# Performance work log

Measured on AMD Instinct MI355X. Metric: run time of the kernel, lower is better.

The kernel has to match this reference:

```python
import jax, jax.numpy as jnp
import numpy as np

A_CUBIC = -0.5  # Keys cubic-convolution parameter (order-3 spline approximation)


def _cubic(t):
    # Keys cubic interpolation kernel, support (-2, 2)
    at = jnp.abs(t)
    at2 = at * at
    at3 = at2 * at
    a = A_CUBIC
    w_inner = (a + 2.0) * at3 - (a + 3.0) * at2 + 1.0          # |t| <= 1
    w_outer = a * at3 - 5.0 * a * at2 + 8.0 * a * at - 4.0 * a  # 1 < |t| < 2
    return jnp.where(at <= 1.0, w_inner, jnp.where(at < 2.0, w_outer, 0.0))


def _spline_upsample_matrix(n_out, n_ctrl):
    # (n_out, n_ctrl) dense weight matrix interpolating control points to the
    # full-resolution axis with the cubic kernel; edge taps clamped (nearest).
    u = jnp.arange(n_out, dtype=jnp.float32) * (n_ctrl - 1) / (n_out - 1)
    i0 = jnp.floor(u).astype(jnp.int32)
    taps = i0[:, None] + jnp.arange(-1, 3)                      # (n_out, 4)
    w = _cubic(u[:, None] - taps.astype(jnp.float32))           # (n_out, 4)
    taps_c = jnp.clip(taps, 0, n_ctrl - 1)
    B = jnp.zeros((n_out, n_ctrl), jnp.float32)
    B = B.at[jnp.arange(n_out)[:, None], taps_c].add(w)
    return B


def _elastic_warp(img, displacement):
    # img: (H, W, C); displacement: (2, 3, 3) control-point displacements (dy, dx)
    H, W, C = img.shape
    By = _spline_upsample_matrix(H, displacement.shape[1])      # (H, 3)
    Bx = _spline_upsample_matrix(W, displacement.shape[2])      # (W, 3)
    disp = jnp.einsum('hy,dyx,wx->dhw', By, displacement, Bx)   # (2, H, W)

    yy = jnp.arange(H, dtype=jnp.float32)[:, None] + disp[0]    # sample coords
    xx = jnp.arange(W, dtype=jnp.float32)[None, :] + disp[1]
    iy0 = jnp.floor(yy).astype(jnp.int32)
    ix0 = jnp.floor(xx).astype(jnp.int32)

    out = jnp.zeros_like(img)
    # 4x4 cubic tap stencil (fixed small loop; each iteration is one full gather)
    for a in range(-1, 3):
        ty = iy0 + a
        wy = _cubic(yy - ty.astype(jnp.float32))                # (H, W)
        tyc = jnp.clip(ty, 0, H - 1)
        for b in range(-1, 3):
            tx = ix0 + b
            wx = _cubic(xx - tx.astype(jnp.float32))            # (H, W)
            txc = jnp.clip(tx, 0, W - 1)
            out = out + (wy * wx)[..., None] * img[tyc, txc]    # gather (H,W,C)
    return out


def setup_inputs() -> dict:
    key = jax.random.key(0)
    k1, k2 = jax.random.split(key)
    H, W, C = 2048, 4096, 3
    inputs = jax.random.normal(k1, (H, W, C), dtype=jnp.float32)
    displacement = jax.random.normal(k2, (2, 3, 3), dtype=jnp.float32)
    return {"inputs": inputs, "displacement": displacement}


def reference(inputs, displacement):
    # module draws displacement ~ N(0,1)*5 internally; externalized here
    return _elastic_warp(inputs, displacement * 5.0)
```

## Files before the change

kernel.cpp:

```cpp
#include <hip/hip_runtime.h>
#include <math.h>

constexpr int H = 2048;
constexpr int W = 4096;
constexpr int RS = W * 3;

__device__ __forceinline__ float k_inner(float t) {
    return fmaf(fmaf(1.5f, t, -2.5f), t * t, 1.0f);
}
__device__ __forceinline__ float k_outer(float t) {
    return fmaf(fmaf(fmaf(-0.5f, t, 2.5f), t, -4.0f), t, 2.0f);
}
__device__ __forceinline__ float cubic_w(float t) {
    float at = fabsf(t);
    if (at <= 1.0f) return k_inner(at);
    if (at < 2.0f)  return k_outer(at);
    return 0.0f;
}

__global__ __launch_bounds__(256, 4)
void elastic_warp_kernel(const float* __restrict__ img,
                         const float* __restrict__ dctrl,
                         float* __restrict__ out) {
    int h = blockIdx.x >> 4;
    int w = ((blockIdx.x & 15) << 8) | threadIdx.x;

    __shared__ float s_cy[6];
    if (threadIdx.x == 0) {
        float u = (float)(2 * h) / (float)(H - 1);
        float i0 = floorf(u);
        float by0 = 0.0f, by1 = 0.0f, by2 = 0.0f;
#pragma unroll
        for (int k = -1; k < 3; ++k) {
            float tap = i0 + (float)k;
            float wt = cubic_w(u - tap);
            int tc = (int)tap;
            tc = tc < 0 ? 0 : (tc > 2 ? 2 : tc);
            if (tc == 0) by0 += wt; else if (tc == 1) by1 += wt; else by2 += wt;
        }
#pragma unroll
        for (int x = 0; x < 3; ++x) {
            s_cy[x]     = 5.0f * (by0 * dctrl[x]     + by1 * dctrl[3 + x]  + by2 * dctrl[6 + x]);
            s_cy[3 + x] = 5.0f * (by0 * dctrl[9 + x] + by1 * dctrl[12 + x] + by2 * dctrl[15 + x]);
        }
    }
    __syncthreads();

    float u = (float)w * (2.0f / 4095.0f);
    bool hiu = u >= 1.0f;
    float s = u - (hiu ? 1.0f : 0.0f);
    float o1 = k_outer(1.0f + s);
    float is = k_inner(s);
    float i1 = k_inner(1.0f - s);
    float o2 = k_outer(2.0f - s);
    float bx0 = hiu ? o1 : (o1 + is);
    float bx1 = hiu ? is : i1;
    float bx2 = hiu ? (i1 + o2) : o2;

    float d0 = s_cy[0] * bx0 + s_cy[1] * bx1 + s_cy[2] * bx2;
    float d1 = s_cy[3] * bx0 + s_cy[4] * bx1 + s_cy[5] * bx2;

    float yy = (float)h + d0;
    float xx = (float)w + d1;
    float iy0f = floorf(yy);
    float ix0f = floorf(xx);
    float fy = yy - iy0f;
    float fx = xx - ix0f;
    int iy0 = (int)iy0f;
    int ix0 = (int)ix0f;

    float wy0 = k_outer(1.0f + fy), wy1 = k_inner(fy), wy2 = k_inner(1.0f - fy), wy3 = k_outer(2.0f - fy);
    float wx0 = k_outer(1.0f + fx), wx1 = k_inner(fx), wx2 = k_inner(1.0f - fx), wx3 = k_outer(2.0f - fx);
    float wy[4] = {wy0, wy1, wy2, wy3};

    float acc0 = 0.0f, acc1 = 0.0f, acc2 = 0.0f;

    bool interior = (iy0 >= 1) & (iy0 <= H - 3) & (ix0 >= 1) & (ix0 <= W - 3);
    if (interior) {
        int off = ((iy0 - 1) * W + (ix0 - 1)) * 3;

        float4 v[4][3];
#pragma unroll
        for (int a = 0; a < 4; ++a) {
            const float4* p = (const float4*)(img + off + a * RS);
            v[a][0] = p[0];
            v[a][1] = p[1];
            v[a][2] = p[2];
        }

#pragma unroll
        for (int a = 0; a < 4; ++a) {
            float q0 = wy[a] * wx0, q1 = wy[a] * wx1, q2 = wy[a] * wx2, q3 = wy[a] * wx3;
            float4 va = v[a][0], vb = v[a][1], vc = v[a][2];
            acc0 = fmaf(q0, va.x, fmaf(q1, va.w, fmaf(q2, vb.z, fmaf(q3, vc.y, acc0))));
            acc1 = fmaf(q0, va.y, fmaf(q1, vb.x, fmaf(q2, vb.w, fmaf(q3, vc.z, acc1))));
            acc2 = fmaf(q0, va.z, fmaf(q1, vb.y, fmaf(q2, vc.x, fmaf(q3, vc.w, acc2))));
        }
    } else {
        float wx[4] = {wx0, wx1, wx2, wx3};
#pragma unroll
        for (int a = 0; a < 4; ++a) {
            int ty = iy0 + a - 1;
            ty = ty < 0 ? 0 : (ty > H - 1 ? H - 1 : ty);
            int rowoff = ty * RS;
            float ay = wy[a];
#pragma unroll
            for (int b = 0; b < 4; ++b) {
                int tx = ix0 + b - 1;
                tx = tx < 0 ? 0 : (tx > W - 1 ? W - 1 : tx);
                float wgt = ay * wx[b];
                const float* p = img + rowoff + tx * 3;
                acc0 += wgt * p[0];
                acc1 += wgt * p[1];
                acc2 += wgt * p[2];
            }
        }
    }

    int oo = (blockIdx.x * 256 + threadIdx.x) * 3;
    out[oo + 0] = acc0;
    out[oo + 1] = acc1;
    out[oo + 2] = acc2;
}

extern "C" void kernel_launch(void* const* d_in, const int* in_sizes, int n_in,
                              void* d_out, int out_size, void* d_ws, size_t ws_size,
                              hipStream_t stream) {
    const float* img   = (const float*)d_in[0];
    const float* dctrl = (const float*)d_in[1];
    float* out = (float*)d_out;

    int blocks = (H * W) / 256;
    elastic_warp_kernel<<<blocks, 256, 0, stream>>>(img, dctrl, out);
}
```

Measured before the change: 66.85 us.

## Process two adjacent pixels per thread sharing a 6x6 stencil load

Each thread now computes two horizontally adjacent output pixels and loads one shared 6-row by 6-pixel window, with per-pixel weights shifted into that window according to the relative offsets. This is meant to cut redundant global loads between overlapping stencils and halve the thread count. The fast path runs only when every lane in the wavefront meets the offset and bounds conditions; otherwise all lanes fall back to two scalar clamped gathers. Output stores become float2 writes. The risks are higher register pressure, since the occupancy hint was dropped from launch bounds, and extra FMAs against zero weights.

```diff
diff --git a/kernel.cpp b/kernel.cpp
--- a/kernel.cpp
+++ b/kernel.cpp
@@ -18,18 +18,42 @@
     return 0.0f;
 }
 
-__global__ __launch_bounds__(256, 4)
+__device__ __forceinline__ void gather_px(const float* __restrict__ img,
+                                          int iy, int ix,
+                                          const float wy[4], const float wx[4],
+                                          float& o0, float& o1, float& o2) {
+    o0 = 0.f; o1 = 0.f; o2 = 0.f;
+#pragma unroll
+    for (int a = 0; a < 4; ++a) {
+        int ty = iy + a - 1;
+        ty = ty < 0 ? 0 : (ty > H - 1 ? H - 1 : ty);
+        int rowoff = ty * RS;
+        float ay = wy[a];
+#pragma unroll
+        for (int b = 0; b < 4; ++b) {
+            int tx = ix + b - 1;
+            tx = tx < 0 ? 0 : (tx > W - 1 ? W - 1 : tx);
+            float wgt = ay * wx[b];
+            const float* p = img + rowoff + tx * 3;
+            o0 += wgt * p[0];
+            o1 += wgt * p[1];
+            o2 += wgt * p[2];
+        }
+    }
+}
+
+__global__ __launch_bounds__(256)
 void elastic_warp_kernel(const float* __restrict__ img,
                          const float* __restrict__ dctrl,
                          float* __restrict__ out) {
-    int h = blockIdx.x >> 4;
-    int w = ((blockIdx.x & 15) << 8) | threadIdx.x;
+    int h  = blockIdx.x >> 3;
+    int x0 = ((blockIdx.x & 7) << 9) | ((int)threadIdx.x << 1);
 
     __shared__ float s_cy[6];
     if (threadIdx.x == 0) {
         float u = (float)(2 * h) / (float)(H - 1);
         float i0 = floorf(u);
-        float by0 = 0.0f, by1 = 0.0f, by2 = 0.0f;
+        float by0 = 0.f, by1 = 0.f, by2 = 0.f;
 #pragma unroll
         for (int k = -1; k < 3; ++k) {
             float tap = i0 + (float)k;
@@ -45,82 +69,118 @@
         }
     }
     __syncthreads();
+    float cy0 = s_cy[0], cy1 = s_cy[1], cy2 = s_cy[2];
+    float cy3 = s_cy[3], cy4 = s_cy[4], cy5 = s_cy[5];
 
-    float u = (float)w * (2.0f / 4095.0f);
-    bool hiu = u >= 1.0f;
-    float s = u - (hiu ? 1.0f : 0.0f);
-    float o1 = k_outer(1.0f + s);
-    float is = k_inner(s);
-    float i1 = k_inner(1.0f - s);
-    float o2 = k_outer(2.0f - s);
-    float bx0 = hiu ? o1 : (o1 + is);
-    float bx1 = hiu ? is : i1;
-    float bx2 = hiu ? (i1 + o2) : o2;
+    float d0[2], d1[2];
+#pragma unroll
+    for (int p = 0; p < 2; ++p) {
+        float u = (float)(x0 + p) * (2.0f / 4095.0f);
+        bool hiu = u >= 1.0f;
+        float s = u - (hiu ? 1.0f : 0.0f);
+        float o1v = k_outer(1.0f + s);
+        float isv = k_inner(s);
+        float i1v = k_inner(1.0f - s);
+        float o2v = k_outer(2.0f - s);
+        float bx0 = hiu ? o1v : (o1v + isv);
+        float bx1 = hiu ? isv : i1v;
+        float bx2 = hiu ? (i1v + o2v) : o2v;
+        d0[p] = cy0 * bx0 + cy1 * bx1 + cy2 * bx2;
+        d1[p] = cy3 * bx0 + cy4 * bx1 + cy5 * bx2;
+    }
 
-    float d0 = s_cy[0] * bx0 + s_cy[1] * bx1 + s_cy[2] * bx2;
-    float d1 = s_cy[3] * bx0 + s_cy[4] * bx1 + s_cy[5] * bx2;
+    float yy0 = (float)h + d0[0],  xx0 = (float)x0 + d1[0];
+    float yy1 = (float)h + d0[1],  xx1 = (float)(x0 + 1) + d1[1];
+    float fly0 = floorf(yy0), flx0 = floorf(xx0);
+    float fly1 = floorf(yy1), flx1 = floorf(xx1);
+    float fy0 = yy0 - fly0, fx0 = xx0 - flx0;
+    float fy1 = yy1 - fly1, fx1 = xx1 - flx1;
+    int iy0 = (int)fly0, ix0 = (int)flx0;
+    int iy1 = (int)fly1, ix1 = (int)flx1;
 
-    float yy = (float)h + d0;
-    float xx = (float)w + d1;
-    float iy0f = floorf(yy);
-    float ix0f = floorf(xx);
-    float fy = yy - iy0f;
-    float fx = xx - ix0f;
-    int iy0 = (int)iy0f;
-    int ix0 = (int)ix0f;
+    float wy0[4] = {k_outer(1.f + fy0), k_inner(fy0), k_inner(1.f - fy0), k_outer(2.f - fy0)};
+    float wx0[4] = {k_outer(1.f + fx0), k_inner(fx0), k_inner(1.f - fx0), k_outer(2.f - fx0)};
+    float wy1[4] = {k_outer(1.f + fy1), k_inner(fy1), k_inner(1.f - fy1), k_outer(2.f - fy1)};
+    float wx1[4] = {k_outer(1.f + fx1), k_inner(fx1), k_inner(1.f - fx1), k_outer(2.f - fx1)};
 
-    float wy0 = k_outer(1.0f + fy), wy1 = k_inner(fy), wy2 = k_inner(1.0f - fy), wy3 = k_outer(2.0f - fy);
-    float wx0 = k_outer(1.0f + fx), wx1 = k_inner(fx), wx2 = k_inner(1.0f - fx), wx3 = k_outer(2.0f - fx);
-    float wy[4] = {wy0, wy1, wy2, wy3};
+    float a0, a1, a2, b0, b1, b2;
 
-    float acc0 = 0.0f, acc1 = 0.0f, acc2 = 0.0f;
+    int e  = ix1 - ix0;
+    int f1 = iy1 - iy0 + 1;
+    bool fast = (iy0 >= 2) & (iy0 <= H - 4) & (ix0 >= 1) & (ix0 <= W - 5) &
+                (e >= 0) & (e <= 2) & (f1 >= 0) & (f1 <= 2);
 
-    bool interior = (iy0 >= 1) & (iy0 <= H - 3) & (ix0 >= 1) & (ix0 <= W - 3);
-    if (interior) {
-        int off = ((iy0 - 1) * W + (ix0 - 1)) * 3;
+    if (__all(fast)) {
+        int br = iy0 - 2;
+        int bc3 = (ix0 - 1) * 3;
 
-        float4 v[4][3];
-#pragma unroll
-        for (int a = 0; a < 4; ++a) {
-            const float4* p = (const float4*)(img + off + a * RS);
-            v[a][0] = p[0];
-            v[a][1] = p[1];
-            v[a][2] = p[2];
-        }
+        bool e0 = (e == 0), e1 = (e == 1);
+        float wx1d[6];
+        wx1d[0] = e0 ? wx1[0] : 0.f;
+        wx1d[1] = e0 ? wx1[1] : (e1 ? wx1[0] : 0.f);
+        wx1d[2] = e0 ? wx1[2] : (e1 ? wx1[1] : wx1[0]);
+        wx1d[3] = e0 ? wx1[3] : (e1 ? wx1[2] : wx1[1]);
+        wx1d[4] = e0 ? 0.f    : (e1 ? wx1[3] : wx1[2]);
+        wx1d[5] = (!e0 && !e1) ? wx1[3] : 0.f;
+
+        bool f0 = (f1 == 0), fo = (f1 == 1);
+        float wr1[6];
+        wr1[0] = f0 ? wy1[0] : 0.f;
+        wr1[1] = f0 ? wy1[1] : (fo ? wy1[0] : 0.f);
+        wr1[2] = f0 ? wy1[2] : (fo ? wy1[1] : wy1[0]);
+        wr1[3] = f0 ? wy1[3] : (fo ? wy1[2] : wy1[1]);
+        wr1[4] = f0 ? 0.f    : (fo ? wy1[3] : wy1[2]);
+        wr1[5] = (!f0 && !fo) ? wy1[3] : 0.f;
+
+        a0 = a1 = a2 = 0.f;
+        b0 = b1 = b2 = 0.f;
 
 #pragma unroll
-        for (int a = 0; a < 4; ++a) {
-            float q0 = wy[a] * wx0, q1 = wy[a] * wx1, q2 = wy[a] * wx2, q3 = wy[a] * wx3;
-            float4 va = v[a][0], vb = v[a][1], vc = v[a][2];
-            acc0 = fmaf(q0, va.x, fmaf(q1, va.w, fmaf(q2, vb.z, fmaf(q3, vc.y, acc0))));
-            acc1 = fmaf(q0, va.y, fmaf(q1, vb.x, fmaf(q2, vb.w, fmaf(q3, vc.z, acc1))));
-            acc2 = fmaf(q0, va.z, fmaf(q1, vb.y, fmaf(q2, vc.x, fmaf(q3, vc.w, acc2))));
+        for (int r = 0; r < 6; ++r) {
+            const float* rp = img + (br + r) * RS + bc3;
+            float4 A = *(const float4*)(rp);
+            float4 B = *(const float4*)(rp + 4);
+            float4 Cc = *(const float4*)(rp + 8);
+            float4 E = *(const float4*)(rp + 12);
+            float2 Dd = *(const float2*)(rp + 16);
+            float v0 = A.x,  v1 = A.y,  v2 = A.z,  v3 = A.w;
+            float v4 = B.x,  v5 = B.y,  v6 = B.z,  v7 = B.w;
+            float v8 = Cc.x, v9 = Cc.y, v10 = Cc.z, v11 = Cc.w;
+            float v12 = E.x, v13 = E.y, v14 = E.z, v15 = E.w;
+            float v16 = Dd.x, v17 = Dd.y;
+
+            float s0 = fmaf(wx1d[0], v0,  fmaf(wx1d[1], v3,  fmaf(wx1d[2], v6,
+                       fmaf(wx1d[3], v9,  fmaf(wx1d[4], v12, wx1d[5] * v15)))));
+            float s1 = fmaf(wx1d[0], v1,  fmaf(wx1d[1], v4,  fmaf(wx1d[2], v7,
+                       fmaf(wx1d[3], v10, fmaf(wx1d[4], v13, wx1d[5] * v16)))));
+            float s2 = fmaf(wx1d[0], v2,  fmaf(wx1d[1], v5,  fmaf(wx1d[2], v8,
+                       fmaf(wx1d[3], v11, fmaf(wx1d[4], v14, wx1d[5] * v17)))));
+            b0 = fmaf(wr1[r], s0, b0);
+            b1 = fmaf(wr1[r], s1, b1);
+            b2 = fmaf(wr1[r], s2, b2);
+
+            if (r >= 1 && r <= 4) {
+                float t0 = fmaf(wx0[0], v0, fmaf(wx0[1], v3, fmaf(wx0[2], v6,  wx0[3] * v9)));
+                float t1 = fmaf(wx0[0], v1, fmaf(wx0[1], v4, fmaf(wx0[2], v7,  wx0[3] * v10)));
+                float t2 = fmaf(wx0[0], v2, fmaf(wx0[1], v5, fmaf(wx0[2], v8,  wx0[3] * v11)));
+                float ay = wy0[r - 1];
+                a0 = fmaf(ay, t0, a0);
+                a1 = fmaf(ay, t1, a1);
+                a2 = fmaf(ay, t2, a2);
+            }
         }
     } else {
-        float wx[4] = {wx0, wx1, wx2, wx3};
-#pragma unroll
-        for (int a = 0; a < 4; ++a) {
-            int ty = iy0 + a - 1;
-            ty = ty < 0 ? 0 : (ty > H - 1 ? H - 1 : ty);
-            int rowoff = ty * RS;
-            float ay = wy[a];
-#pragma unroll
-            for (int b = 0; b < 4; ++b) {
-                int tx = ix0 + b - 1;
-                tx = tx < 0 ? 0 : (tx > W - 1 ? W - 1 : tx);
-                float wgt = ay * wx[b];
-                const float* p = img + rowoff + tx * 3;
-                acc0 += wgt * p[0];
-                acc1 += wgt * p[1];
-                acc2 += wgt * p[2];
-            }
-        }
+        gather_px(img, iy0, ix0, wy0, wx0, a0, a1, a2);
+        gather_px(img, iy1, ix1, wy1, wx1, b0, b1, b2);
     }
 
-    int oo = (blockIdx.x * 256 + threadIdx.x) * 3;
-    out[oo + 0] = acc0;
-    out[oo + 1] = acc1;
-    out[oo + 2] = acc2;
+    int oo = (h * W + x0) * 3;
+    float2 w01 = {a0, a1};
+    float2 w23 = {a2, b0};
+    float2 w45 = {b1, b2};
+    *(float2*)(out + oo)     = w01;
+    *(float2*)(out + oo + 2) = w23;
+    *(float2*)(out + oo + 4) = w45;
 }
 
 extern "C" void kernel_launch(void* const* d_in, const int* in_sizes, int n_in,
@@ -130,6 +190,6 @@
     const float* dctrl = (const float*)d_in[1];
     float* out = (float*)d_out;
 
-    int blocks = (H * W) / 256;
+    int blocks = H * (W / 512);
     elastic_warp_kernel<<<blocks, 256, 0, stream>>>(img, dctrl, out);
 }
```

Result: slower. 101.4 us (+51.7%).

## Stage 2D image window in LDS and gather cubic taps from shared memory

Applied to the files above, without the earlier changes.

Reshapes blocks from 1x256 rows to 64x4 tiles and cooperatively loads a 12-row by 72-pixel window of the image into shared memory, sized around the block's base displacement. Each thread then reads its 4x4 stencil from LDS instead of issuing unaligned global float4 loads, exploiting the smooth displacement field to reuse neighbouring pixels. A block-wide vote falls back to the clamped global path when any tap lies outside the window. This adds two extra barriers and shared-memory traffic, and lowers occupancy through the launch-bounds change and the LDS footprint.

```diff
diff --git a/kernel.cpp b/kernel.cpp
--- a/kernel.cpp
+++ b/kernel.cpp
@@ -4,6 +4,10 @@
 constexpr int H = 2048;
 constexpr int W = 4096;
 constexpr int RS = W * 3;
+
+constexpr int WIN_ROWS = 12;
+constexpr int WIN_DW   = 216;
+constexpr int WIN_STRIDE = 220;
 
 __device__ __forceinline__ float k_inner(float t) {
     return fmaf(fmaf(1.5f, t, -2.5f), t * t, 1.0f);
@@ -18,34 +22,26 @@
     return 0.0f;
 }
 
-__global__ __launch_bounds__(256, 4)
-void elastic_warp_kernel(const float* __restrict__ img,
-                         const float* __restrict__ dctrl,
-                         float* __restrict__ out) {
-    int h = blockIdx.x >> 4;
-    int w = ((blockIdx.x & 15) << 8) | threadIdx.x;
+__device__ __forceinline__ void row_cy(int h, const float* __restrict__ dctrl, float cy[6]) {
+    float u = (float)(2 * h) / (float)(H - 1);
+    float i0 = floorf(u);
+    float by0 = 0.f, by1 = 0.f, by2 = 0.f;
+#pragma unroll
+    for (int k = -1; k < 3; ++k) {
+        float tap = i0 + (float)k;
+        float wt = cubic_w(u - tap);
+        int tc = (int)tap;
+        tc = tc < 0 ? 0 : (tc > 2 ? 2 : tc);
+        if (tc == 0) by0 += wt; else if (tc == 1) by1 += wt; else by2 += wt;
+    }
+#pragma unroll
+    for (int x = 0; x < 3; ++x) {
+        cy[x]     = 5.0f * (by0 * dctrl[x]     + by1 * dctrl[3 + x]  + by2 * dctrl[6 + x]);
+        cy[3 + x] = 5.0f * (by0 * dctrl[9 + x] + by1 * dctrl[12 + x] + by2 * dctrl[15 + x]);
+    }
+}
 
-    __shared__ float s_cy[6];
-    if (threadIdx.x == 0) {
-        float u = (float)(2 * h) / (float)(H - 1);
-        float i0 = floorf(u);
-        float by0 = 0.0f, by1 = 0.0f, by2 = 0.0f;
-#pragma unroll
-        for (int k = -1; k < 3; ++k) {
-            float tap = i0 + (float)k;
-            float wt = cubic_w(u - tap);
-            int tc = (int)tap;
-            tc = tc < 0 ? 0 : (tc > 2 ? 2 : tc);
-            if (tc == 0) by0 += wt; else if (tc == 1) by1 += wt; else by2 += wt;
-        }
-#pragma unroll
-        for (int x = 0; x < 3; ++x) {
-            s_cy[x]     = 5.0f * (by0 * dctrl[x]     + by1 * dctrl[3 + x]  + by2 * dctrl[6 + x]);
-            s_cy[3 + x] = 5.0f * (by0 * dctrl[9 + x] + by1 * dctrl[12 + x] + by2 * dctrl[15 + x]);
-        }
-    }
-    __syncthreads();
-
+__device__ __forceinline__ void bx3(int w, float& b0, float& b1, float& b2) {
     float u = (float)w * (2.0f / 4095.0f);
     bool hiu = u >= 1.0f;
     float s = u - (hiu ? 1.0f : 0.0f);
@@ -53,50 +49,100 @@
     float is = k_inner(s);
     float i1 = k_inner(1.0f - s);
     float o2 = k_outer(2.0f - s);
-    float bx0 = hiu ? o1 : (o1 + is);
-    float bx1 = hiu ? is : i1;
-    float bx2 = hiu ? (i1 + o2) : o2;
+    b0 = hiu ? o1 : (o1 + is);
+    b1 = hiu ? is : i1;
+    b2 = hiu ? (i1 + o2) : o2;
+}
 
-    float d0 = s_cy[0] * bx0 + s_cy[1] * bx1 + s_cy[2] * bx2;
-    float d1 = s_cy[3] * bx0 + s_cy[4] * bx1 + s_cy[5] * bx2;
+__global__ __launch_bounds__(256)
+void elastic_warp_kernel(const float* __restrict__ img,
+                         const float* __restrict__ dctrl,
+                         float* __restrict__ out) {
+    int x0 = blockIdx.x << 6;
+    int y0 = blockIdx.y << 2;
+    int t = threadIdx.x;
+    int r = t >> 6;
+    int w = x0 + (t & 63);
+    int h = y0 + r;
+
+    __shared__ float s_cy[4][6];
+    __shared__ int   s_base[2];
+    __shared__ int   s_flag[4];
+    __shared__ float s_win[WIN_ROWS][WIN_STRIDE];
+
+    if (t < 4) {
+        float cy[6];
+        row_cy(y0 + t, dctrl, cy);
+#pragma unroll
+        for (int j = 0; j < 6; ++j) s_cy[t][j] = cy[j];
+        if (t == 0) {
+            float b0, b1, b2; bx3(x0, b0, b1, b2);
+            float d0 = cy[0]*b0 + cy[1]*b1 + cy[2]*b2;
+            float d1 = cy[3]*b0 + cy[4]*b1 + cy[5]*b2;
+            s_base[0] = (int)floorf((float)y0 + d0);
+            s_base[1] = (int)floorf((float)x0 + d1);
+        }
+    }
+    __syncthreads();
+
+    float cy0 = s_cy[r][0], cy1 = s_cy[r][1], cy2 = s_cy[r][2];
+    float cy3 = s_cy[r][3], cy4 = s_cy[r][4], cy5 = s_cy[r][5];
+    int base_iy = s_base[0], base_ix = s_base[1];
+
+    float bx0, bx1, bx2; bx3(w, bx0, bx1, bx2);
+    float d0 = cy0*bx0 + cy1*bx1 + cy2*bx2;
+    float d1 = cy3*bx0 + cy4*bx1 + cy5*bx2;
 
     float yy = (float)h + d0;
     float xx = (float)w + d1;
-    float iy0f = floorf(yy);
-    float ix0f = floorf(xx);
-    float fy = yy - iy0f;
-    float fx = xx - ix0f;
-    int iy0 = (int)iy0f;
-    int ix0 = (int)ix0f;
+    float fly = floorf(yy), flx = floorf(xx);
+    float fy = yy - fly, fx = xx - flx;
+    int iy0 = (int)fly, ix0 = (int)flx;
+
+    int yb = base_iy - 2;
+    int xb = (base_ix - 2) & ~3;
+
+    int ry0 = iy0 - 1 - yb;
+    int cxp = ix0 - 1 - xb;
+
+    bool uok = (yb >= 0) & (yb + WIN_ROWS - 1 <= H - 1) & (xb >= 0) & (xb + 71 <= W - 1);
+    bool lok = (ry0 >= 0) & (ry0 <= 8) & (cxp >= 0) & (cxp <= 68);
+    int wflag = __all(uok & lok);
+    if ((t & 63) == 0) s_flag[t >> 6] = wflag;
+    __syncthreads();
+    bool fast = s_flag[0] && s_flag[1] && s_flag[2] && s_flag[3];
 
     float wy0 = k_outer(1.0f + fy), wy1 = k_inner(fy), wy2 = k_inner(1.0f - fy), wy3 = k_outer(2.0f - fy);
     float wx0 = k_outer(1.0f + fx), wx1 = k_inner(fx), wx2 = k_inner(1.0f - fx), wx3 = k_outer(2.0f - fx);
-    float wy[4] = {wy0, wy1, wy2, wy3};
 
-    float acc0 = 0.0f, acc1 = 0.0f, acc2 = 0.0f;
+    float acc0 = 0.f, acc1 = 0.f, acc2 = 0.f;
 
-    bool interior = (iy0 >= 1) & (iy0 <= H - 3) & (ix0 >= 1) & (ix0 <= W - 3);
-    if (interior) {
-        int off = ((iy0 - 1) * W + (ix0 - 1)) * 3;
+    if (fast) {
+        const float* gbase = img + yb * RS + xb * 3;
+#pragma unroll
+        for (int it = 0; it < 3; ++it) {
+            int idx = t + (it << 8);
+            if (idx < 648) {
+                int row = idx / 54;
+                int c4  = idx - row * 54;
+                float4 v = *(const float4*)(gbase + row * RS + (c4 << 2));
+                *(float4*)&s_win[row][c4 << 2] = v;
+            }
+        }
+        __syncthreads();
 
-        float4 v[4][3];
+        int cxd = cxp * 3;
+        float wyA[4] = {wy0, wy1, wy2, wy3};
 #pragma unroll
         for (int a = 0; a < 4; ++a) {
-            const float4* p = (const float4*)(img + off + a * RS);
-            v[a][0] = p[0];
-            v[a][1] = p[1];
-            v[a][2] = p[2];
-        }
-
-#pragma unroll
-        for (int a = 0; a < 4; ++a) {
-            float q0 = wy[a] * wx0, q1 = wy[a] * wx1, q2 = wy[a] * wx2, q3 = wy[a] * wx3;
-            float4 va = v[a][0], vb = v[a][1], vc = v[a][2];
-            acc0 = fmaf(q0, va.x, fmaf(q1, va.w, fmaf(q2, vb.z, fmaf(q3, vc.y, acc0))));
-            acc1 = fmaf(q0, va.y, fmaf(q1, vb.x, fmaf(q2, vb.w, fmaf(q3, vc.z, acc1))));
-            acc2 = fmaf(q0, va.z, fmaf(q1, vb.y, fmaf(q2, vc.x, fmaf(q3, vc.w, acc2))));
+            const float* p = &s_win[ry0 + a][cxd];
+            float q0 = wyA[a] * wx0, q1 = wyA[a] * wx1, q2 = wyA[a] * wx2, q3 = wyA[a] * wx3;
+            acc0 = fmaf(q0, p[0], fmaf(q1, p[3], fmaf(q2, p[6],  fmaf(q3, p[9],  acc0))));
+            acc1 = fmaf(q0, p[1], fmaf(q1, p[4], fmaf(q2, p[7],  fmaf(q3, p[10], acc1))));
+            acc2 = fmaf(q0, p[2], fmaf(q1, p[5], fmaf(q2, p[8],  fmaf(q3, p[11], acc2))));
         }
     } else {
+        float wy[4] = {wy0, wy1, wy2, wy3};
         float wx[4] = {wx0, wx1, wx2, wx3};
 #pragma unroll
         for (int a = 0; a < 4; ++a) {
@@ -117,7 +163,7 @@
         }
     }
 
-    int oo = (blockIdx.x * 256 + threadIdx.x) * 3;
+    int oo = (h * W + w) * 3;
     out[oo + 0] = acc0;
     out[oo + 1] = acc1;
     out[oo + 2] = acc2;
@@ -130,6 +176,6 @@
     const float* dctrl = (const float*)d_in[1];
     float* out = (float*)d_out;
 
-    int blocks = (H * W) / 256;
-    elastic_warp_kernel<<<blocks, 256, 0, stream>>>(img, dctrl, out);
+    dim3 grid(W / 64, H / 4);
+    elastic_warp_kernel<<<grid, 256, 0, stream>>>(img, dctrl, out);
 }
```

After: 72.87 us. 1.09x slower.

## Process vertical pixel pairs per thread sharing five source rows in 2D tiles

Applied to the files above, without the earlier changes.

Each thread now computes two vertically adjacent output pixels over four column iterations inside a 64x32 2D block tile. When both pixels share the same integer x and consecutive integer y, it loads five source rows instead of eight, so loads are reused. Outputs use nontemporal stores, and the edge path moves into a noinline helper. The trade-offs are higher register pressure, the dropped occupancy hint in launch bounds, and less coalesced stores because only 16 lanes cover contiguous x.

```diff
diff --git a/kernel.cpp b/kernel.cpp
--- a/kernel.cpp
+++ b/kernel.cpp
@@ -18,18 +18,57 @@
     return 0.0f;
 }
 
-__global__ __launch_bounds__(256, 4)
+__device__ __noinline__ void gather_px(const float* __restrict__ img,
+                                       int iy, int ix,
+                                       float fy, float fx,
+                                       float& o0, float& o1, float& o2) {
+    float wy[4] = {k_outer(1.f + fy), k_inner(fy), k_inner(1.f - fy), k_outer(2.f - fy)};
+    float wx[4] = {k_outer(1.f + fx), k_inner(fx), k_inner(1.f - fx), k_outer(2.f - fx)};
+    o0 = 0.f; o1 = 0.f; o2 = 0.f;
+#pragma unroll
+    for (int a = 0; a < 4; ++a) {
+        int ty = iy + a - 1;
+        ty = ty < 0 ? 0 : (ty > H - 1 ? H - 1 : ty);
+        int rowoff = ty * RS;
+        float ay = wy[a];
+#pragma unroll
+        for (int b = 0; b < 4; ++b) {
+            int tx = ix + b - 1;
+            tx = tx < 0 ? 0 : (tx > W - 1 ? W - 1 : tx);
+            float wgt = ay * wx[b];
+            const float* p = img + rowoff + tx * 3;
+            o0 += wgt * p[0];
+            o1 += wgt * p[1];
+            o2 += wgt * p[2];
+        }
+    }
+}
+
+#define ROWDOT(va, vb, vc, wxA, wxB, wxC, wxD, T0, T1, T2)                         \
+    T0 = fmaf(wxA, va.x, fmaf(wxB, va.w, fmaf(wxC, vb.z, wxD * vc.y)));            \
+    T1 = fmaf(wxA, va.y, fmaf(wxB, vb.x, fmaf(wxC, vb.w, wxD * vc.z)));            \
+    T2 = fmaf(wxA, va.z, fmaf(wxB, vb.y, fmaf(wxC, vc.x, wxD * vc.w)));
+
+__global__ __launch_bounds__(256)
 void elastic_warp_kernel(const float* __restrict__ img,
                          const float* __restrict__ dctrl,
                          float* __restrict__ out) {
-    int h = blockIdx.x >> 4;
-    int w = ((blockIdx.x & 15) << 8) | threadIdx.x;
+    int x0r = blockIdx.x << 6;
+    int y0  = blockIdx.y << 5;
 
-    __shared__ float s_cy[6];
-    if (threadIdx.x == 0) {
-        float u = (float)(2 * h) / (float)(H - 1);
+    int t = threadIdx.x;
+    int lane = t & 63;
+    int wave = t >> 6;
+    int xi = lane & 15;
+    int gi = lane >> 4;
+    int r0 = ((wave << 2) + gi) << 1;
+
+    __shared__ float s_cy[32][6];
+    if (t < 32) {
+        int hh = y0 + t;
+        float u = (float)(2 * hh) / (float)(H - 1);
         float i0 = floorf(u);
-        float by0 = 0.0f, by1 = 0.0f, by2 = 0.0f;
+        float by0 = 0.f, by1 = 0.f, by2 = 0.f;
 #pragma unroll
         for (int k = -1; k < 3; ++k) {
             float tap = i0 + (float)k;
@@ -40,87 +79,103 @@
         }
 #pragma unroll
         for (int x = 0; x < 3; ++x) {
-            s_cy[x]     = 5.0f * (by0 * dctrl[x]     + by1 * dctrl[3 + x]  + by2 * dctrl[6 + x]);
-            s_cy[3 + x] = 5.0f * (by0 * dctrl[9 + x] + by1 * dctrl[12 + x] + by2 * dctrl[15 + x]);
+            s_cy[t][x]     = 5.0f * (by0 * dctrl[x]     + by1 * dctrl[3 + x]  + by2 * dctrl[6 + x]);
+            s_cy[t][3 + x] = 5.0f * (by0 * dctrl[9 + x] + by1 * dctrl[12 + x] + by2 * dctrl[15 + x]);
         }
     }
     __syncthreads();
 
-    float u = (float)w * (2.0f / 4095.0f);
-    bool hiu = u >= 1.0f;
-    float s = u - (hiu ? 1.0f : 0.0f);
-    float o1 = k_outer(1.0f + s);
-    float is = k_inner(s);
-    float i1 = k_inner(1.0f - s);
-    float o2 = k_outer(2.0f - s);
-    float bx0 = hiu ? o1 : (o1 + is);
-    float bx1 = hiu ? is : i1;
-    float bx2 = hiu ? (i1 + o2) : o2;
+    int h0 = y0 + r0;
+    float cyA0 = s_cy[r0][0], cyA1 = s_cy[r0][1], cyA2 = s_cy[r0][2];
+    float cyA3 = s_cy[r0][3], cyA4 = s_cy[r0][4], cyA5 = s_cy[r0][5];
+    float cyB0 = s_cy[r0+1][0], cyB1 = s_cy[r0+1][1], cyB2 = s_cy[r0+1][2];
+    float cyB3 = s_cy[r0+1][3], cyB4 = s_cy[r0+1][4], cyB5 = s_cy[r0+1][5];
+    int rowbase0 = (h0 * W) * 3;
 
-    float d0 = s_cy[0] * bx0 + s_cy[1] * bx1 + s_cy[2] * bx2;
-    float d1 = s_cy[3] * bx0 + s_cy[4] * bx1 + s_cy[5] * bx2;
+#pragma unroll
+    for (int it = 0; it < 4; ++it) {
+        int w = x0r + (it << 4) + xi;
 
-    float yy = (float)h + d0;
-    float xx = (float)w + d1;
-    float iy0f = floorf(yy);
-    float ix0f = floorf(xx);
-    float fy = yy - iy0f;
-    float fx = xx - ix0f;
-    int iy0 = (int)iy0f;
-    int ix0 = (int)ix0f;
+        float u = (float)w * (2.0f / 4095.0f);
+        bool hiu = u >= 1.0f;
+        float s = u - (hiu ? 1.0f : 0.0f);
+        float o1 = k_outer(1.0f + s);
+        float is = k_inner(s);
+        float i1 = k_inner(1.0f - s);
+        float o2 = k_outer(2.0f - s);
+        float bx0 = hiu ? o1 : (o1 + is);
+        float bx1 = hiu ? is : i1;
+        float bx2 = hiu ? (i1 + o2) : o2;
 
-    float wy0 = k_outer(1.0f + fy), wy1 = k_inner(fy), wy2 = k_inner(1.0f - fy), wy3 = k_outer(2.0f - fy);
-    float wx0 = k_outer(1.0f + fx), wx1 = k_inner(fx), wx2 = k_inner(1.0f - fx), wx3 = k_outer(2.0f - fx);
-    float wy[4] = {wy0, wy1, wy2, wy3};
+        float d0a = cyA0 * bx0 + cyA1 * bx1 + cyA2 * bx2;
+        float d1a = cyA3 * bx0 + cyA4 * bx1 + cyA5 * bx2;
+        float d0b = cyB0 * bx0 + cyB1 * bx1 + cyB2 * bx2;
+        float d1b = cyB3 * bx0 + cyB4 * bx1 + cyB5 * bx2;
 
-    float acc0 = 0.0f, acc1 = 0.0f, acc2 = 0.0f;
+        float yy0 = (float)h0 + d0a,        xx0 = (float)w + d1a;
+        float yy1 = (float)(h0 + 1) + d0b,  xx1 = (float)w + d1b;
+        float fly0 = floorf(yy0), flx0 = floorf(xx0);
+        float fly1 = floorf(yy1), flx1 = floorf(xx1);
+        float fy0 = yy0 - fly0, fx0 = xx0 - flx0;
+        float fy1 = yy1 - fly1, fx1 = xx1 - flx1;
+        int iy0 = (int)fly0, ix0 = (int)flx0;
+        int iy1 = (int)fly1, ix1 = (int)flx1;
 
-    bool interior = (iy0 >= 1) & (iy0 <= H - 3) & (ix0 >= 1) & (ix0 <= W - 3);
-    if (interior) {
-        int off = ((iy0 - 1) * W + (ix0 - 1)) * 3;
+        float a0 = 0.f, a1 = 0.f, a2 = 0.f;
+        float b0 = 0.f, b1 = 0.f, b2 = 0.f;
 
-        float4 v[4][3];
-#pragma unroll
-        for (int a = 0; a < 4; ++a) {
-            const float4* p = (const float4*)(img + off + a * RS);
-            v[a][0] = p[0];
-            v[a][1] = p[1];
-            v[a][2] = p[2];
+        bool ok = (iy0 >= 1) & (iy0 <= H - 5) & (ix0 >= 1) & (ix0 <= W - 3) &
+                  (iy1 == iy0 + 1) & (ix1 == ix0);
+
+        if (ok) {
+            int off = ((iy0 - 1) * W + (ix0 - 1)) * 3;
+            const float* p0 = img + off;
+            const float* p1 = p0 + RS;
+            const float* p2 = p1 + RS;
+            const float* p3 = p2 + RS;
+            const float* p4 = p3 + RS;
+            float4 v0a = ((const float4*)p0)[0], v0b = ((const float4*)p0)[1], v0c = ((const float4*)p0)[2];
+            float4 v1a = ((const float4*)p1)[0], v1b = ((const float4*)p1)[1], v1c = ((const float4*)p1)[2];
+            float4 v2a = ((const float4*)p2)[0], v2b = ((const float4*)p2)[1], v2c = ((const float4*)p2)[2];
+            float4 v3a = ((const float4*)p3)[0], v3b = ((const float4*)p3)[1], v3c = ((const float4*)p3)[2];
+            float4 v4a = ((const float4*)p4)[0], v4b = ((const float4*)p4)[1], v4c = ((const float4*)p4)[2];
+
+            float wyA0 = k_outer(1.f + fy0), wyA1 = k_inner(fy0), wyA2 = k_inner(1.f - fy0), wyA3 = k_outer(2.f - fy0);
+            float wxA0 = k_outer(1.f + fx0), wxA1 = k_inner(fx0), wxA2 = k_inner(1.f - fx0), wxA3 = k_outer(2.f - fx0);
+            float wyB0 = k_outer(1.f + fy1), wyB1 = k_inner(fy1), wyB2 = k_inner(1.f - fy1), wyB3 = k_outer(2.f - fy1);
+            float wxB0 = k_outer(1.f + fx1), wxB1 = k_inner(fx1), wxB2 = k_inner(1.f - fx1), wxB3 = k_outer(2.f - fx1);
+
+            float t0, t1, t2;
+            ROWDOT(v0a, v0b, v0c, wxA0, wxA1, wxA2, wxA3, t0, t1, t2)
+            a0 = wyA0 * t0; a1 = wyA0 * t1; a2 = wyA0 * t2;
+            ROWDOT(v1a, v1b, v1c, wxA0, wxA1, wxA2, wxA3, t0, t1, t2)
+            a0 = fmaf(wyA1, t0, a0); a1 = fmaf(wyA1, t1, a1); a2 = fmaf(wyA1, t2, a2);
+            ROWDOT(v2a, v2b, v2c, wxA0, wxA1, wxA2, wxA3, t0, t1, t2)
+            a0 = fmaf(wyA2, t0, a0); a1 = fmaf(wyA2, t1, a1); a2 = fmaf(wyA2, t2, a2);
+            ROWDOT(v3a, v3b, v3c, wxA0, wxA1, wxA2, wxA3, t0, t1, t2)
+            a0 = fmaf(wyA3, t0, a0); a1 = fmaf(wyA3, t1, a1); a2 = fmaf(wyA3, t2, a2);
+            ROWDOT(v1a, v1b, v1c, wxB0, wxB1, wxB2, wxB3, t0, t1, t2)
+            b0 = wyB0 * t0; b1 = wyB0 * t1; b2 = wyB0 * t2;
+            ROWDOT(v2a, v2b, v2c, wxB0, wxB1, wxB2, wxB3, t0, t1, t2)
+            b0 = fmaf(wyB1, t0, b0); b1 = fmaf(wyB1, t1, b1); b2 = fmaf(wyB1, t2, b2);
+            ROWDOT(v3a, v3b, v3c, wxB0, wxB1, wxB2, wxB3, t0, t1, t2)
+            b0 = fmaf(wyB2, t0, b0); b1 = fmaf(wyB2, t1, b1); b2 = fmaf(wyB2, t2, b2);
+            ROWDOT(v4a, v4b, v4c, wxB0, wxB1, wxB2, wxB3, t0, t1, t2)
+            b0 = fmaf(wyB3, t0, b0); b1 = fmaf(wyB3, t1, b1); b2 = fmaf(wyB3, t2, b2);
+        }
+        if (!ok) {
+            gather_px(img, iy0, ix0, fy0, fx0, a0, a1, a2);
+            gather_px(img, iy1, ix1, fy1, fx1, b0, b1, b2);
         }
 
-#pragma unroll
-        for (int a = 0; a < 4; ++a) {
-            float q0 = wy[a] * wx0, q1 = wy[a] * wx1, q2 = wy[a] * wx2, q3 = wy[a] * wx3;
-            float4 va = v[a][0], vb = v[a][1], vc = v[a][2];
-            acc0 = fmaf(q0, va.x, fmaf(q1, va.w, fmaf(q2, vb.z, fmaf(q3, vc.y, acc0))));
-            acc1 = fmaf(q0, va.y, fmaf(q1, vb.x, fmaf(q2, vb.w, fmaf(q3, vc.z, acc1))));
-            acc2 = fmaf(q0, va.z, fmaf(q1, vb.y, fmaf(q2, vc.x, fmaf(q3, vc.w, acc2))));
-        }
-    } else {
-        float wx[4] = {wx0, wx1, wx2, wx3};
-#pragma unroll
-        for (int a = 0; a < 4; ++a) {
-            int ty = iy0 + a - 1;
-            ty = ty < 0 ? 0 : (ty > H - 1 ? H - 1 : ty);
-            int rowoff = ty * RS;
-            float ay = wy[a];
-#pragma unroll
-            for (int b = 0; b < 4; ++b) {
-                int tx = ix0 + b - 1;
-                tx = tx < 0 ? 0 : (tx > W - 1 ? W - 1 : tx);
-                float wgt = ay * wx[b];
-                const float* p = img + rowoff + tx * 3;
-                acc0 += wgt * p[0];
-                acc1 += wgt * p[1];
-                acc2 += wgt * p[2];
-            }
-        }
+        int oo = rowbase0 + w * 3;
+        __builtin_nontemporal_store(a0, out + oo);
+        __builtin_nontemporal_store(a1, out + oo + 1);
+        __builtin_nontemporal_store(a2, out + oo + 2);
+        __builtin_nontemporal_store(b0, out + oo + RS);
+        __builtin_nontemporal_store(b1, out + oo + RS + 1);
+        __builtin_nontemporal_store(b2, out + oo + RS + 2);
     }
-
-    int oo = (blockIdx.x * 256 + threadIdx.x) * 3;
-    out[oo + 0] = acc0;
-    out[oo + 1] = acc1;
-    out[oo + 2] = acc2;
 }
 
 extern "C" void kernel_launch(void* const* d_in, const int* in_sizes, int n_in,
@@ -130,6 +185,6 @@
     const float* dctrl = (const float*)d_in[1];
     float* out = (float*)d_out;
 
-    int blocks = (H * W) / 256;
-    elastic_warp_kernel<<<blocks, 256, 0, stream>>>(img, dctrl, out);
+    dim3 grid(W / 64, H / 32);
+    elastic_warp_kernel<<<grid, 256, 0, stream>>>(img, dctrl, out);
 }
```

Measured after the change: 163.6 us. 2.45x slower.
